# Kernel optimization log

Hardware: AMD Instinct MI355X
Metric: run time of the kernel (lower is better)

## Reference

```python
import jax, jax.numpy as jnp
import numpy as np

T, B, D, H, L, O = 800, 32, 440, 1024, 4, 2000
EPS = 1e-5

def _bn(x, g, b, m, v):
    return (x - m) * jax.lax.rsqrt(v + EPS) * g + b

def setup_inputs() -> dict:
    key = jax.random.key(0)
    ks = jax.random.split(key, 12)
    s = 0.02
    return {
        "xs": jax.random.normal(ks[0], (T, B, D), dtype=jnp.float32),
        "w0": jax.random.normal(ks[1], (2 * H, D), dtype=jnp.float32) * s,
        "wr": jax.random.normal(ks[2], (L - 1, 2 * H, H), dtype=jnp.float32) * s,
        "bnz_g": jnp.ones((L, H), jnp.float32),
        "bnz_b": jnp.zeros((L, H), jnp.float32),
        "bnz_m": jax.random.normal(ks[3], (L, H), dtype=jnp.float32) * 0.1,
        "bnz_v": jax.random.uniform(ks[4], (L, H), dtype=jnp.float32) + 0.5,
        "bnc_g": jnp.ones((L, H), jnp.float32),
        "bnc_b": jnp.zeros((L, H), jnp.float32),
        "bnc_m": jax.random.normal(ks[5], (L, H), dtype=jnp.float32) * 0.1,
        "bnc_v": jax.random.uniform(ks[6], (L, H), dtype=jnp.float32) + 0.5,
        "wf": jax.random.normal(ks[7], (O, H), dtype=jnp.float32) * 0.003,
        "bnf_g": jnp.ones((O,), jnp.float32),
        "bnf_b": jnp.zeros((O,), jnp.float32),
        "bnf_m": jax.random.normal(ks[8], (O,), dtype=jnp.float32) * 0.1,
        "bnf_v": jax.random.uniform(ks[9], (O,), dtype=jnp.float32) + 0.5,
    }

def reference(xs, w0, wr, bnz_g, bnz_b, bnz_m, bnz_v, bnc_g, bnc_b, bnc_m, bnc_v, wf, bnf_g, bnf_b, bnf_m, bnf_v):
    x = xs  # [T,B,feat]
    for i in range(L):
        W = w0 if i == 0 else wr[i - 1]
        ws = jnp.einsum('tbd,hd->tbh', x, W)          # [T,B,2H]
        wz, wc = jnp.split(ws, 2, axis=-1)
        z = jax.nn.sigmoid(_bn(wz, bnz_g[i], bnz_b[i], bnz_m[i], bnz_v[i]))
        c = jax.nn.relu(_bn(wc, bnc_g[i], bnc_b[i], bnc_m[i], bnc_v[i]))
        def step(h, zc):
            z_t, c_t = zc
            h = (1.0 - z_t) * c_t + z_t * h
            return h, h
        _, hs = jax.lax.scan(step, jnp.zeros((B, H), x.dtype), (z, c))
        x = hs  # [T,B,H]
    out = jnp.einsum('tbh,oh->tbo', x, wf).reshape(T * B, O)
    out = _bn(out, bnf_g, bnf_b, bnf_m, bnf_v)
    return jax.nn.log_softmax(out, axis=1)
```

## Files before the change

kernel.cpp:

```cpp
#include <hip/hip_runtime.h>
#include <math.h>
#include <stdint.h>

#define T_ 800
#define B_ 32
#define D_ 440
#define DP_ 448
#define H_ 1024
#define L_ 4
#define O_ 2000
#define OP_ 2048
#define EPS_ 1e-5f
#define M_ (T_ * B_)
#define BH_ (B_ * H_)
#define NC_ 16
#define TC_ (T_ / NC_)

#define BM2 128
#define BN2 256
#define BK2 32

typedef __attribute__((ext_vector_type(8))) short bf16x8;
typedef __attribute__((ext_vector_type(4))) float f32x4;

__device__ inline float b2f(unsigned short u) {
    union { unsigned int i; float f; } v; v.i = ((unsigned int)u) << 16; return v.f;
}
__device__ inline unsigned short f2b(float f) {
    unsigned int x = __float_as_uint(f);
    return (unsigned short)((x + 0x7FFFu + ((x >> 16) & 1u)) >> 16);
}

__global__ void bn_prep(const float* __restrict__ g, const float* __restrict__ b,
                        const float* __restrict__ m, const float* __restrict__ v,
                        float* __restrict__ scale, float* __restrict__ bias,
                        int nsrc, int ndst)
{
    int i = blockIdx.x * 256 + threadIdx.x;
    if (i >= ndst) return;
    if (i < nsrc) {
        float s = g[i] * rsqrtf(v[i] + EPS_);
        scale[i] = s;
        bias[i] = fmaf(-m[i], s, b[i]);
    } else {
        scale[i] = 0.f;
        bias[i] = 0.f;
    }
}

__global__ void cvt_pad8(const float* __restrict__ src, unsigned short* __restrict__ dst,
                         int Rs, int Cs, int Cd, int total8)
{
    int i = blockIdx.x * 256 + threadIdx.x;
    if (i >= total8) return;
    const int c8 = Cd >> 3;
    int r = i / c8, c = (i - r * c8) << 3;
    ushort4 lo, hi;
    if (r < Rs && c < Cs) {
        const float4 a = *(const float4*)(src + (size_t)r * Cs + c);
        const float4 b = *(const float4*)(src + (size_t)r * Cs + c + 4);
        lo = make_ushort4(f2b(a.x), f2b(a.y), f2b(a.z), f2b(a.w));
        hi = make_ushort4(f2b(b.x), f2b(b.y), f2b(b.z), f2b(b.w));
    } else {
        lo = make_ushort4(0, 0, 0, 0);
        hi = make_ushort4(0, 0, 0, 0);
    }
    unsigned short* d = dst + (size_t)r * Cd + c;
    *(ushort4*)d = lo;
    *(ushort4*)(d + 4) = hi;
}


#define GLDS16(src, dst) __builtin_amdgcn_global_load_lds( \
    (const __attribute__((address_space(1))) unsigned int*)(src), \
    (__attribute__((address_space(3))) unsigned int*)(dst), 16, 0, 0)

#define SBAR() __builtin_amdgcn_s_barrier()
#define LGKM0() do { asm volatile("s_waitcnt lgkmcnt(0)" ::: "memory"); \
                     __builtin_amdgcn_sched_barrier(0); } while (0)

__global__ __launch_bounds__(256, 2) void gemm_bf16(
    const unsigned short* __restrict__ A, const unsigned short* __restrict__ Wt,
    int K, int mode,
    unsigned short* __restrict__ zout, unsigned short* __restrict__ cout,
    const float* __restrict__ zscale, const float* __restrict__ zbias,
    const float* __restrict__ cscale, const float* __restrict__ cbias,
    unsigned short* __restrict__ fout,
    const float* __restrict__ fscale, const float* __restrict__ fbias)
{
    __shared__ unsigned short As[2][128 * 32];
    __shared__ unsigned short Bs[2][256 * 32];

    const int tid = threadIdx.x;
    const int lane = tid & 63;
    const int wid = tid >> 6;

    const int g = blockIdx.x;
    const int n_t = (g >> 3) & 7;
    const int m_t = ((g >> 6) << 3) | (g & 7);
    const int m0 = m_t * BM2;
    const int n0 = n_t * BN2;

    const int srow = lane >> 2;
    const int scol = (lane & 3) * 8;

    const unsigned short* aE = A + (size_t)(m0 + wid * 16 + srow) * K + scol;
    const unsigned short* aL = A + (size_t)(m0 + 64 + wid * 16 + srow) * K + scol;
    const unsigned short* bS0 = Wt + (size_t)(n0 + wid * 64 + srow * 4 + 0) * K + scol;
    const unsigned short* bS1 = Wt + (size_t)(n0 + wid * 64 + srow * 4 + 1) * K + scol;
    const unsigned short* bS2 = Wt + (size_t)(n0 + wid * 64 + srow * 4 + 2) * K + scol;
    const unsigned short* bS3 = Wt + (size_t)(n0 + wid * 64 + srow * 4 + 3) * K + scol;

    const int lsAE = wid * 512;
    const int lsAL = (4 + wid) * 512;
    const int lsB0 = (wid * 4 + 0) * 512;
    const int lsB1 = (wid * 4 + 1) * 512;
    const int lsB2 = (wid * 4 + 2) * 512;
    const int lsB3 = (wid * 4 + 3) * 512;

    const int fr = lane & 15;
    const int q = lane >> 4;
    const int rdc = q * 8;

    f32x4 acc[8][4];
    #pragma unroll
    for (int i = 0; i < 8; i++)
        #pragma unroll
        for (int j = 0; j < 4; j++)
            acc[i][j] = (f32x4){0.f, 0.f, 0.f, 0.f};

    bf16x8 af[4], bfv[4];

    const int nT = K / BK2;

    GLDS16(aE,  &As[0][lsAE]);
    GLDS16(bS0, &Bs[0][lsB0]); GLDS16(bS1, &Bs[0][lsB1]);
    GLDS16(bS2, &Bs[0][lsB2]); GLDS16(bS3, &Bs[0][lsB3]);
    GLDS16(aL,  &As[0][lsAL]);
    if (nT > 1) {
        GLDS16(aE + BK2,  &As[1][lsAE]);
        GLDS16(bS0 + BK2, &Bs[1][lsB0]); GLDS16(bS1 + BK2, &Bs[1][lsB1]);
        GLDS16(bS2 + BK2, &Bs[1][lsB2]); GLDS16(bS3 + BK2, &Bs[1][lsB3]);
        asm volatile("s_waitcnt vmcnt(6)" ::: "memory");
    } else {
        asm volatile("s_waitcnt vmcnt(1)" ::: "memory");
    }
    SBAR();

#define MFMA16(MBASE) do { \
    __builtin_amdgcn_s_setprio(1); \
    _Pragma("unroll") \
    for (int m_ = 0; m_ < 4; ++m_) \
        _Pragma("unroll") \
        for (int n_ = 0; n_ < 4; ++n_) \
            acc[MBASE + m_][n_] = __builtin_amdgcn_mfma_f32_16x16x32_bf16( \
                af[m_], bfv[n_], acc[MBASE + m_][n_], 0, 0, 0); \
    __builtin_amdgcn_s_setprio(0); \
} while (0)

    for (int t = 0; t < nT; ++t) {
        const int cur = t & 1, nxt = cur ^ 1;
        const unsigned short* Ac = As[cur];
        const unsigned short* Bc = Bs[cur] + wid * (64 * 32);
        const int kL = (t + 1) * BK2;
        const int kE = (t + 2) * BK2;

        #pragma unroll
        for (int m_ = 0; m_ < 4; ++m_)
            af[m_] = *(const bf16x8*)(Ac + (m_ * 16 + fr) * 32 + rdc);
        #pragma unroll
        for (int n_ = 0; n_ < 4; ++n_)
            bfv[n_] = *(const bf16x8*)(Bc + (n_ * 16 + fr) * 32 + rdc);
        if (t + 1 < nT) {
            GLDS16(aL + kL, &As[nxt][lsAL]);
        }
        SBAR();
        LGKM0();
        MFMA16(0);
        if (t + 1 < nT) {
            asm volatile("s_waitcnt vmcnt(6)" ::: "memory");
        } else {
            asm volatile("s_waitcnt vmcnt(0)" ::: "memory");
        }
        SBAR();

        #pragma unroll
        for (int m_ = 0; m_ < 4; ++m_)
            af[m_] = *(const bf16x8*)(Ac + ((4 + m_) * 16 + fr) * 32 + rdc);
        if (t + 2 < nT) {
            GLDS16(aE + kE,  &As[cur][lsAE]);
            GLDS16(bS0 + kE, &Bs[cur][lsB0]); GLDS16(bS1 + kE, &Bs[cur][lsB1]);
            GLDS16(bS2 + kE, &Bs[cur][lsB2]); GLDS16(bS3 + kE, &Bs[cur][lsB3]);
        }
        SBAR();
        LGKM0();
        MFMA16(4);
        if (t + 2 < nT) {
            asm volatile("s_waitcnt vmcnt(6)" ::: "memory");
        } else if (t + 1 < nT) {
            asm volatile("s_waitcnt vmcnt(1)" ::: "memory");
        } else {
            asm volatile("s_waitcnt vmcnt(0)" ::: "memory");
        }
        SBAR();
    }

#undef MFMA16

    const int colb = n0 + wid * 64 + fr * 4;
    const int rbase = m0 + q * 4;

    if (mode == 0) {
        const bool isz = (n0 < H_);
        const float* sc = isz ? zscale : cscale;
        const float* bi = isz ? zbias : cbias;
        unsigned short* dst = isz ? zout : cout;
        const int npb = isz ? colb : colb - H_;
        const float4 s4 = *(const float4*)(sc + npb);
        const float4 b4 = *(const float4*)(bi + npb);
        #pragma unroll
        for (int m = 0; m < 8; ++m)
            #pragma unroll
            for (int r = 0; r < 4; ++r) {
                const int mm = rbase + m * 16 + r;
                float v0 = fmaf(acc[m][0][r], s4.x, b4.x);
                float v1 = fmaf(acc[m][1][r], s4.y, b4.y);
                float v2 = fmaf(acc[m][2][r], s4.z, b4.z);
                float v3 = fmaf(acc[m][3][r], s4.w, b4.w);
                if (isz) {
                    v0 = __builtin_amdgcn_rcpf(1.f + __expf(-v0));
                    v1 = __builtin_amdgcn_rcpf(1.f + __expf(-v1));
                    v2 = __builtin_amdgcn_rcpf(1.f + __expf(-v2));
                    v3 = __builtin_amdgcn_rcpf(1.f + __expf(-v3));
                } else {
                    v0 = fmaxf(v0, 0.f); v1 = fmaxf(v1, 0.f);
                    v2 = fmaxf(v2, 0.f); v3 = fmaxf(v3, 0.f);
                }
                ushort4 pk = make_ushort4(f2b(v0), f2b(v1), f2b(v2), f2b(v3));
                *(ushort4*)(dst + (size_t)mm * H_ + npb) = pk;
            }
    } else {
        const float4 s4 = *(const float4*)(fscale + colb);
        const float4 b4 = *(const float4*)(fbias + colb);
        #pragma unroll
        for (int m = 0; m < 8; ++m)
            #pragma unroll
            for (int r = 0; r < 4; ++r) {
                const int mm = rbase + m * 16 + r;
                ushort4 pk = make_ushort4(
                    f2b(fmaf(acc[m][0][r], s4.x, b4.x)),
                    f2b(fmaf(acc[m][1][r], s4.y, b4.y)),
                    f2b(fmaf(acc[m][2][r], s4.z, b4.z)),
                    f2b(fmaf(acc[m][3][r], s4.w, b4.w)));
                *(ushort4*)(fout + (size_t)mm * OP_ + colb) = pk;
            }
    }
}

__global__ __launch_bounds__(256) void scan_pass1(
    const unsigned short* __restrict__ z, const unsigned short* __restrict__ c,
    float* __restrict__ H0, float* __restrict__ P)
{
    const int k = blockIdx.y;
    const int e2 = blockIdx.x * 256 + threadIdx.x;
    float h0 = 0.f, h1 = 0.f, p0 = 1.f, p1 = 1.f;
    size_t off = ((size_t)k * TC_ * BH_ + 2 * e2) >> 1;
    const unsigned int* z32 = (const unsigned int*)z;
    const unsigned int* c32 = (const unsigned int*)c;
    #pragma unroll 5
    for (int t = 0; t < TC_; ++t) {
        unsigned int zz = z32[off], cc = c32[off];
        float z0 = b2f((unsigned short)zz), z1 = b2f((unsigned short)(zz >> 16));
        float c0 = b2f((unsigned short)cc), c1 = b2f((unsigned short)(cc >> 16));
        h0 = fmaf(z0, h0 - c0, c0);  p0 *= z0;
        h1 = fmaf(z1, h1 - c1, c1);  p1 *= z1;
        off += BH_ / 2;
    }
    *(float2*)(H0 + (size_t)k * BH_ + 2 * e2) = make_float2(h0, h1);
    *(float2*)(P  + (size_t)k * BH_ + 2 * e2) = make_float2(p0, p1);
}

__global__ __launch_bounds__(256) void scan_pass2(
    const unsigned short* __restrict__ z, const unsigned short* __restrict__ c,
    const float* __restrict__ H0, const float* __restrict__ P,
    unsigned short* __restrict__ x)
{
    const int k = blockIdx.y;
    const int e2 = blockIdx.x * 256 + threadIdx.x;
    float h0 = 0.f, h1 = 0.f;
    for (int j = 0; j < k; ++j) {
        float2 pj = *(const float2*)(P  + (size_t)j * BH_ + 2 * e2);
        float2 hj = *(const float2*)(H0 + (size_t)j * BH_ + 2 * e2);
        h0 = fmaf(pj.x, h0, hj.x);
        h1 = fmaf(pj.y, h1, hj.y);
    }
    size_t off = ((size_t)k * TC_ * BH_ + 2 * e2) >> 1;
    const unsigned int* z32 = (const unsigned int*)z;
    const unsigned int* c32 = (const unsigned int*)c;
    unsigned int* x32 = (unsigned int*)x;
    #pragma unroll 5
    for (int t = 0; t < TC_; ++t) {
        unsigned int zz = z32[off], cc = c32[off];
        float z0 = b2f((unsigned short)zz), z1 = b2f((unsigned short)(zz >> 16));
        float c0 = b2f((unsigned short)cc), c1 = b2f((unsigned short)(cc >> 16));
        h0 = fmaf(z0, h0 - c0, c0);
        h1 = fmaf(z1, h1 - c1, c1);
        x32[off] = (unsigned int)f2b(h0) | ((unsigned int)f2b(h1) << 16);
        off += BH_ / 2;
    }
}

__global__ __launch_bounds__(256) void logsoftmax_kernel(
    const unsigned short* __restrict__ lg, float* __restrict__ out)
{
    const int row = blockIdx.x;
    const unsigned short* p = lg + (size_t)row * OP_;
    float* po = out + (size_t)row * O_;
    const int tid = threadIdx.x;

    float v[8];
    float mx = -1e30f;
    #pragma unroll
    for (int j = 0; j < 8; j++) {
        int col = tid + j * 256;
        v[j] = (col < O_) ? b2f(p[col]) : -1e30f;
        mx = fmaxf(mx, v[j]);
    }
    #pragma unroll
    for (int o = 32; o > 0; o >>= 1) mx = fmaxf(mx, __shfl_down(mx, o));
    __shared__ float smax[4];
    __shared__ float ssum[4];
    const int lane = tid & 63, wid = tid >> 6;
    if (lane == 0) smax[wid] = mx;
    __syncthreads();
    mx = fmaxf(fmaxf(smax[0], smax[1]), fmaxf(smax[2], smax[3]));

    float s = 0.f;
    #pragma unroll
    for (int j = 0; j < 8; j++) {
        int col = tid + j * 256;
        if (col < O_) s += expf(v[j] - mx);
    }
    #pragma unroll
    for (int o = 32; o > 0; o >>= 1) s += __shfl_down(s, o);
    if (lane == 0) ssum[wid] = s;
    __syncthreads();
    s = ssum[0] + ssum[1] + ssum[2] + ssum[3];
    const float lse = mx + logf(s);

    #pragma unroll
    for (int j = 0; j < 8; j++) {
        int col = tid + j * 256;
        if (col < O_) po[col] = v[j] - lse;
    }
}

extern "C" void kernel_launch(void* const* d_in, const int* in_sizes, int n_in,
                              void* d_out, int out_size, void* d_ws, size_t ws_size,
                              hipStream_t stream)
{
    (void)in_sizes; (void)n_in; (void)out_size; (void)ws_size;

    const float* xs    = (const float*)d_in[0];
    const float* w0    = (const float*)d_in[1];
    const float* wr    = (const float*)d_in[2];
    const float* bnz_g = (const float*)d_in[3];
    const float* bnz_b = (const float*)d_in[4];
    const float* bnz_m = (const float*)d_in[5];
    const float* bnz_v = (const float*)d_in[6];
    const float* bnc_g = (const float*)d_in[7];
    const float* bnc_b = (const float*)d_in[8];
    const float* bnc_m = (const float*)d_in[9];
    const float* bnc_v = (const float*)d_in[10];
    const float* wf    = (const float*)d_in[11];
    const float* bnf_g = (const float*)d_in[12];
    const float* bnf_b = (const float*)d_in[13];
    const float* bnf_m = (const float*)d_in[14];
    const float* bnf_v = (const float*)d_in[15];
    float* out = (float*)d_out;

    unsigned short* p = (unsigned short*)d_ws;
    unsigned short* xbuf  = p;  p += (size_t)M_ * H_;
    unsigned short* x0buf = p;  p += (size_t)M_ * DP_;
    unsigned short* zbuf  = p;  p += (size_t)M_ * H_;
    unsigned short* cbuf  = p;  p += (size_t)M_ * H_;
    unsigned short* w0p   = p;  p += (size_t)(2 * H_) * DP_;
    unsigned short* wrp   = p;  p += (size_t)(L_ - 1) * (2 * H_) * H_;
    unsigned short* wfp   = p;  p += (size_t)OP_ * H_;
    unsigned short* lbuf  = p;  p += (size_t)M_ * OP_;
    float* fp = (float*)p;
    float* zs = fp;  fp += L_ * H_;
    float* zb = fp;  fp += L_ * H_;
    float* cs = fp;  fp += L_ * H_;
    float* cb = fp;  fp += L_ * H_;
    float* fs = fp;  fp += OP_;
    float* fb = fp;  fp += OP_;
    float* sH0 = fp; fp += NC_ * BH_;
    float* sP  = fp;

    dim3 blk(256);
    bn_prep<<<(L_ * H_ + 255) / 256, blk, 0, stream>>>(bnz_g, bnz_b, bnz_m, bnz_v, zs, zb, L_ * H_, L_ * H_);
    bn_prep<<<(L_ * H_ + 255) / 256, blk, 0, stream>>>(bnc_g, bnc_b, bnc_m, bnc_v, cs, cb, L_ * H_, L_ * H_);
    bn_prep<<<(OP_ + 255) / 256, blk, 0, stream>>>(bnf_g, bnf_b, bnf_m, bnf_v, fs, fb, O_, OP_);

    {
        int t0 = M_ * DP_ / 8;
        cvt_pad8<<<(t0 + 255) / 256, blk, 0, stream>>>(xs, x0buf, M_, D_, DP_, t0);
        int t1 = 2 * H_ * DP_ / 8;
        cvt_pad8<<<(t1 + 255) / 256, blk, 0, stream>>>(w0, w0p, 2 * H_, D_, DP_, t1);
        int t2 = (L_ - 1) * 2 * H_ * H_ / 8;
        cvt_pad8<<<(t2 + 255) / 256, blk, 0, stream>>>(wr, wrp, (L_ - 1) * 2 * H_, H_, H_, t2);
        int t3 = OP_ * H_ / 8;
        cvt_pad8<<<(t3 + 255) / 256, blk, 0, stream>>>(wf, wfp, O_, H_, H_, t3);
    }

    dim3 blk2(256);
    dim3 grid2((M_ / BM2) * ((2 * H_) / BN2));
    dim3 sgrid1(BH_ / 512, NC_ - 1);
    dim3 sgrid2(BH_ / 512, NC_);
    for (int layer = 0; layer < L_; ++layer) {
        const unsigned short* Ain = (layer == 0) ? x0buf : xbuf;
        const unsigned short* W   = (layer == 0) ? w0p : (wrp + (size_t)(layer - 1) * (2 * H_) * H_);
        const int K               = (layer == 0) ? DP_ : H_;
        gemm_bf16<<<grid2, blk2, 0, stream>>>(Ain, W, K, 0,
            zbuf, cbuf,
            zs + layer * H_, zb + layer * H_, cs + layer * H_, cb + layer * H_,
            nullptr, nullptr, nullptr);
        scan_pass1<<<sgrid1, blk, 0, stream>>>(zbuf, cbuf, sH0, sP);
        scan_pass2<<<sgrid2, blk, 0, stream>>>(zbuf, cbuf, sH0, sP, xbuf);
    }

    dim3 gridf((M_ / BM2) * (OP_ / BN2));
    gemm_bf16<<<gridf, blk2, 0, stream>>>(xbuf, wfp, H_, 1,
        nullptr, nullptr, nullptr, nullptr, nullptr, nullptr,
        lbuf, fs, fb);

    logsoftmax_kernel<<<M_, blk, 0, stream>>>(lbuf, out);
}
```

Before: 1.073 ms.

## Load GEMM B fragments directly to registers, swizzle A LDS layout

The bf16 GEMM no longer stages the weight tile through LDS. Each wave loads its B MFMA fragments straight from global memory into registers, double-buffered across K tiles. The A tile keeps its LDS double buffer but gains an XOR swizzle to cut bank conflicts, and the main loop is simplified to one barrier and a full vmcnt(0) wait per tile. This removes LDS traffic and capacity for B, which could allow more overlap, but it adds uncoalesced strided global reads and a full memory wait every iteration. The epilogue also switches from packed 4-wide stores to scalar bf16 stores at stride-16 columns.

```diff
diff --git a/kernel.cpp b/kernel.cpp
--- a/kernel.cpp
+++ b/kernel.cpp
@@ -76,8 +76,11 @@
     (__attribute__((address_space(3))) unsigned int*)(dst), 16, 0, 0)
 
 #define SBAR() __builtin_amdgcn_s_barrier()
+#define FENCE() __builtin_amdgcn_sched_barrier(0)
 #define LGKM0() do { asm volatile("s_waitcnt lgkmcnt(0)" ::: "memory"); \
                      __builtin_amdgcn_sched_barrier(0); } while (0)
+#define VM0() do { asm volatile("s_waitcnt vmcnt(0)" ::: "memory"); \
+                   __builtin_amdgcn_sched_barrier(0); } while (0)
 
 __global__ __launch_bounds__(256, 2) void gemm_bf16(
     const unsigned short* __restrict__ A, const unsigned short* __restrict__ Wt,
@@ -89,7 +92,6 @@
     const float* __restrict__ fscale, const float* __restrict__ fbias)
 {
     __shared__ unsigned short As[2][128 * 32];
-    __shared__ unsigned short Bs[2][256 * 32];
 
     const int tid = threadIdx.x;
     const int lane = tid & 63;
@@ -102,25 +104,21 @@
     const int n0 = n_t * BN2;
 
     const int srow = lane >> 2;
-    const int scol = (lane & 3) * 8;
+    const int scol = ((lane & 3) * 8) ^ (((srow >> 1) & 3) << 3);
 
     const unsigned short* aE = A + (size_t)(m0 + wid * 16 + srow) * K + scol;
     const unsigned short* aL = A + (size_t)(m0 + 64 + wid * 16 + srow) * K + scol;
-    const unsigned short* bS0 = Wt + (size_t)(n0 + wid * 64 + srow * 4 + 0) * K + scol;
-    const unsigned short* bS1 = Wt + (size_t)(n0 + wid * 64 + srow * 4 + 1) * K + scol;
-    const unsigned short* bS2 = Wt + (size_t)(n0 + wid * 64 + srow * 4 + 2) * K + scol;
-    const unsigned short* bS3 = Wt + (size_t)(n0 + wid * 64 + srow * 4 + 3) * K + scol;
-
     const int lsAE = wid * 512;
     const int lsAL = (4 + wid) * 512;
-    const int lsB0 = (wid * 4 + 0) * 512;
-    const int lsB1 = (wid * 4 + 1) * 512;
-    const int lsB2 = (wid * 4 + 2) * 512;
-    const int lsB3 = (wid * 4 + 3) * 512;
 
     const int fr = lane & 15;
     const int q = lane >> 4;
-    const int rdc = q * 8;
+    const int rdc = (q * 8) ^ (((fr >> 1) & 3) << 3);
+
+    const unsigned short* bP[4];
+    #pragma unroll
+    for (int n_ = 0; n_ < 4; ++n_)
+        bP[n_] = Wt + (size_t)(n0 + wid * 64 + n_ * 16 + fr) * K + q * 8;
 
     f32x4 acc[8][4];
     #pragma unroll
@@ -129,85 +127,67 @@
         for (int j = 0; j < 4; j++)
             acc[i][j] = (f32x4){0.f, 0.f, 0.f, 0.f};
 
-    bf16x8 af[4], bfv[4];
+    bf16x8 bA[4], bB[4];
 
     const int nT = K / BK2;
 
-    GLDS16(aE,  &As[0][lsAE]);
-    GLDS16(bS0, &Bs[0][lsB0]); GLDS16(bS1, &Bs[0][lsB1]);
-    GLDS16(bS2, &Bs[0][lsB2]); GLDS16(bS3, &Bs[0][lsB3]);
-    GLDS16(aL,  &As[0][lsAL]);
-    if (nT > 1) {
-        GLDS16(aE + BK2,  &As[1][lsAE]);
-        GLDS16(bS0 + BK2, &Bs[1][lsB0]); GLDS16(bS1 + BK2, &Bs[1][lsB1]);
-        GLDS16(bS2 + BK2, &Bs[1][lsB2]); GLDS16(bS3 + BK2, &Bs[1][lsB3]);
-        asm volatile("s_waitcnt vmcnt(6)" ::: "memory");
-    } else {
-        asm volatile("s_waitcnt vmcnt(1)" ::: "memory");
-    }
+    GLDS16(aE, &As[0][lsAE]);
+    GLDS16(aL, &As[0][lsAL]);
+    FENCE();
+    #pragma unroll
+    for (int n_ = 0; n_ < 4; ++n_)
+        bA[n_] = *(const bf16x8*)(bP[n_]);
+    FENCE();
+    VM0();
     SBAR();
 
-#define MFMA16(MBASE) do { \
+#define MFMA_HALF(MBASE, AFR, BREG) do { \
     __builtin_amdgcn_s_setprio(1); \
     _Pragma("unroll") \
     for (int m_ = 0; m_ < 4; ++m_) \
         _Pragma("unroll") \
         for (int n_ = 0; n_ < 4; ++n_) \
             acc[MBASE + m_][n_] = __builtin_amdgcn_mfma_f32_16x16x32_bf16( \
-                af[m_], bfv[n_], acc[MBASE + m_][n_], 0, 0, 0); \
+                AFR[m_], BREG[n_], acc[MBASE + m_][n_], 0, 0, 0); \
     __builtin_amdgcn_s_setprio(0); \
 } while (0)
 
-    for (int t = 0; t < nT; ++t) {
-        const int cur = t & 1, nxt = cur ^ 1;
-        const unsigned short* Ac = As[cur];
-        const unsigned short* Bc = Bs[cur] + wid * (64 * 32);
-        const int kL = (t + 1) * BK2;
-        const int kE = (t + 2) * BK2;
-
-        #pragma unroll
-        for (int m_ = 0; m_ < 4; ++m_)
-            af[m_] = *(const bf16x8*)(Ac + (m_ * 16 + fr) * 32 + rdc);
-        #pragma unroll
-        for (int n_ = 0; n_ < 4; ++n_)
-            bfv[n_] = *(const bf16x8*)(Bc + (n_ * 16 + fr) * 32 + rdc);
-        if (t + 1 < nT) {
-            GLDS16(aL + kL, &As[nxt][lsAL]);
-        }
-        SBAR();
-        LGKM0();
-        MFMA16(0);
-        if (t + 1 < nT) {
-            asm volatile("s_waitcnt vmcnt(6)" ::: "memory");
-        } else {
-            asm volatile("s_waitcnt vmcnt(0)" ::: "memory");
-        }
-        SBAR();
-
-        #pragma unroll
-        for (int m_ = 0; m_ < 4; ++m_)
-            af[m_] = *(const bf16x8*)(Ac + ((4 + m_) * 16 + fr) * 32 + rdc);
-        if (t + 2 < nT) {
-            GLDS16(aE + kE,  &As[cur][lsAE]);
-            GLDS16(bS0 + kE, &Bs[cur][lsB0]); GLDS16(bS1 + kE, &Bs[cur][lsB1]);
-            GLDS16(bS2 + kE, &Bs[cur][lsB2]); GLDS16(bS3 + kE, &Bs[cur][lsB3]);
-        }
-        SBAR();
-        LGKM0();
-        MFMA16(4);
-        if (t + 2 < nT) {
-            asm volatile("s_waitcnt vmcnt(6)" ::: "memory");
-        } else if (t + 1 < nT) {
-            asm volatile("s_waitcnt vmcnt(1)" ::: "memory");
-        } else {
-            asm volatile("s_waitcnt vmcnt(0)" ::: "memory");
-        }
-        SBAR();
-    }
-
-#undef MFMA16
-
-    const int colb = n0 + wid * 64 + fr * 4;
+#define TILE_BODY(CUR, NXT, BUSE, BLOAD, KNXT, COND) do { \
+    const unsigned short* Ac = As[CUR]; \
+    if (COND) { \
+        GLDS16(aE + (KNXT), &As[NXT][lsAE]); \
+        GLDS16(aL + (KNXT), &As[NXT][lsAL]); \
+    } \
+    FENCE(); \
+    if (COND) { \
+        _Pragma("unroll") \
+        for (int n_ = 0; n_ < 4; ++n_) \
+            BLOAD[n_] = *(const bf16x8*)(bP[n_] + (KNXT)); \
+    } \
+    FENCE(); \
+    bf16x8 af1[4], af2[4]; \
+    _Pragma("unroll") \
+    for (int m_ = 0; m_ < 4; ++m_) { \
+        af1[m_] = *(const bf16x8*)(Ac + (m_ * 16 + fr) * 32 + rdc); \
+        af2[m_] = *(const bf16x8*)(Ac + ((4 + m_) * 16 + fr) * 32 + rdc); \
+    } \
+    FENCE(); \
+    LGKM0(); \
+    MFMA_HALF(0, af1, BUSE); \
+    MFMA_HALF(4, af2, BUSE); \
+    VM0(); \
+    SBAR(); \
+} while (0)
+
+    for (int t = 0; t < nT; t += 2) {
+        TILE_BODY(0, 1, bA, bB, (t + 1) * BK2, true);
+        TILE_BODY(1, 0, bB, bA, (t + 2) * BK2, (t + 2 < nT));
+    }
+
+#undef TILE_BODY
+#undef MFMA_HALF
+
+    const int cb = n0 + wid * 64 + fr;
     const int rbase = m0 + q * 4;
 
     if (mode == 0) {
@@ -215,44 +195,43 @@
         const float* sc = isz ? zscale : cscale;
         const float* bi = isz ? zbias : cbias;
         unsigned short* dst = isz ? zout : cout;
-        const int npb = isz ? colb : colb - H_;
-        const float4 s4 = *(const float4*)(sc + npb);
-        const float4 b4 = *(const float4*)(bi + npb);
+        const int cbp = isz ? cb : cb - H_;
+        float s4[4], b4[4];
+        #pragma unroll
+        for (int n_ = 0; n_ < 4; ++n_) {
+            s4[n_] = sc[cbp + n_ * 16];
+            b4[n_] = bi[cbp + n_ * 16];
+        }
         #pragma unroll
         for (int m = 0; m < 8; ++m)
             #pragma unroll
             for (int r = 0; r < 4; ++r) {
                 const int mm = rbase + m * 16 + r;
-                float v0 = fmaf(acc[m][0][r], s4.x, b4.x);
-                float v1 = fmaf(acc[m][1][r], s4.y, b4.y);
-                float v2 = fmaf(acc[m][2][r], s4.z, b4.z);
-                float v3 = fmaf(acc[m][3][r], s4.w, b4.w);
-                if (isz) {
-                    v0 = __builtin_amdgcn_rcpf(1.f + __expf(-v0));
-                    v1 = __builtin_amdgcn_rcpf(1.f + __expf(-v1));
-                    v2 = __builtin_amdgcn_rcpf(1.f + __expf(-v2));
-                    v3 = __builtin_amdgcn_rcpf(1.f + __expf(-v3));
-                } else {
-                    v0 = fmaxf(v0, 0.f); v1 = fmaxf(v1, 0.f);
-                    v2 = fmaxf(v2, 0.f); v3 = fmaxf(v3, 0.f);
+                #pragma unroll
+                for (int n_ = 0; n_ < 4; ++n_) {
+                    float v = fmaf(acc[m][n_][r], s4[n_], b4[n_]);
+                    if (isz) v = __builtin_amdgcn_rcpf(1.f + __expf(-v));
+                    else     v = fmaxf(v, 0.f);
+                    dst[(size_t)mm * H_ + cbp + n_ * 16] = f2b(v);
                 }
-                ushort4 pk = make_ushort4(f2b(v0), f2b(v1), f2b(v2), f2b(v3));
-                *(ushort4*)(dst + (size_t)mm * H_ + npb) = pk;
             }
     } else {
-        const float4 s4 = *(const float4*)(fscale + colb);
-        const float4 b4 = *(const float4*)(fbias + colb);
+        float s4[4], b4[4];
+        #pragma unroll
+        for (int n_ = 0; n_ < 4; ++n_) {
+            s4[n_] = fscale[cb + n_ * 16];
+            b4[n_] = fbias[cb + n_ * 16];
+        }
         #pragma unroll
         for (int m = 0; m < 8; ++m)
             #pragma unroll
             for (int r = 0; r < 4; ++r) {
                 const int mm = rbase + m * 16 + r;
-                ushort4 pk = make_ushort4(
-                    f2b(fmaf(acc[m][0][r], s4.x, b4.x)),
-                    f2b(fmaf(acc[m][1][r], s4.y, b4.y)),
-                    f2b(fmaf(acc[m][2][r], s4.z, b4.z)),
-                    f2b(fmaf(acc[m][3][r], s4.w, b4.w)));
-                *(ushort4*)(fout + (size_t)mm * OP_ + colb) = pk;
+                #pragma unroll
+                for (int n_ = 0; n_ < 4; ++n_) {
+                    float v = fmaf(acc[m][n_][r], s4[n_], b4[n_]);
+                    fout[(size_t)mm * OP_ + cb + n_ * 16] = f2b(v);
+                }
             }
     }
 }
```

After: 1.198 ms. 11.7% more time.
